# Kernel tuning notes

Measured on AMD Instinct MI355X. Metric: run time of the kernel, lower is better.

## Reference

```python
import jax, jax.numpy as jnp
import numpy as np
import math

HEAD_DIM = 128
NUM_Q_HEAD = 32
NUM_KV_HEAD = 8
WINDOW = 512
CAP = 30.0
CLIP_LO, CLIP_HI = -0.03, 1.03
EPS = 1e-5
SCALE = 1.0 / math.sqrt(HEAD_DIM)
B, S = 2, 2048


def group_rms_norm(x, w, group_size, eps):
    # x: [B, S, hidden]; normalize each contiguous group of size group_size
    Bx, Sx, H = x.shape
    ng = H // group_size
    xg = x.reshape(Bx, Sx, ng, group_size)
    inv = jax.lax.rsqrt(jnp.mean(xg * xg, axis=-1, keepdims=True) + eps)
    return (xg * inv).reshape(Bx, Sx, H) * w


def setup_inputs() -> dict:
    key = jax.random.key(0)
    kq, kk, kv, kw1, kw2 = jax.random.split(key, 5)
    q = jax.random.normal(kq, (B, S, NUM_Q_HEAD, HEAD_DIM), dtype=jnp.float32)
    k = jax.random.normal(kk, (B, S, NUM_KV_HEAD, HEAD_DIM), dtype=jnp.float32)
    v = jax.random.normal(kv, (B, S, NUM_KV_HEAD, HEAD_DIM), dtype=jnp.float32)
    # GroupRMSNorm weights, init uniform in (-1, 1)
    q_norm_w = jax.random.uniform(kw1, (NUM_Q_HEAD * HEAD_DIM,), dtype=jnp.float32, minval=-1.0, maxval=1.0)
    kv_norm_w = jax.random.uniform(kw2, (NUM_KV_HEAD * HEAD_DIM,), dtype=jnp.float32, minval=-1.0, maxval=1.0)
    return {"q": q, "k": k, "v": v, "q_norm_w": q_norm_w, "kv_norm_w": kv_norm_w}


def reference(q, k, v, q_norm_w, kv_norm_w):
    Bq, Sq, Hq, D = q.shape
    Sk = k.shape[1]
    # QK GroupRMSNorm over flattened hidden dim, group_size = head_dim
    qn = group_rms_norm(q.reshape(Bq, Sq, Hq * D), q_norm_w, HEAD_DIM, EPS).reshape(q.shape)
    kn = group_rms_norm(k.reshape(Bq, Sk, NUM_KV_HEAD * D), kv_norm_w, HEAD_DIM, EPS).reshape(k.shape)
    # GQA: repeat_interleave kv heads along head axis
    rep = Hq // NUM_KV_HEAD
    kr = jnp.repeat(kn, rep, axis=2)  # [B, Sk, Hq, D]
    vr = jnp.repeat(v, rep, axis=2)
    # scores: [B, Hq, Sq, Sk]
    scores = jnp.einsum("bqhd,bkhd->bhqk", qn, kr) * SCALE
    scores = CAP * jnp.tanh(scores / CAP)  # softmax capping
    # sliding-window + causal mask: allowed iff i - WINDOW <= j <= i (offset = Sk - Sq = 0)
    offset = Sk - Sq
    i = jnp.arange(Sq)[:, None] + offset
    j = jnp.arange(Sk)[None, :]
    allowed = (j <= i) & (j >= i - WINDOW)
    scores = jnp.where(allowed, scores, -jnp.inf)
    probs = jax.nn.softmax(scores, axis=-1)
    probs = jnp.nan_to_num(probs, nan=0.0)
    # softmax clipping
    probs = jnp.clip((CLIP_HI - CLIP_LO) * probs + CLIP_LO, 0.0, 1.0)
    out = jnp.einsum("bhqk,bkhd->bqhd", probs, vr)
    return out
```

## Files before the change

### kernel.cpp

```cpp
#include <hip/hip_runtime.h>

#define SEQ 2048
#define DD 128
#define HQ 32
#define HKV 8
#define WIN 512

typedef unsigned short u16;
typedef unsigned int u32;
typedef __attribute__((ext_vector_type(8))) short bf16x8;
typedef __attribute__((ext_vector_type(4))) float f32x4;
typedef __attribute__((ext_vector_type(2))) float f32x2;

#define SBAR() asm volatile("s_barrier" ::: "memory")
#define WAITV0() asm volatile("s_waitcnt vmcnt(0)" ::: "memory")

__device__ __forceinline__ u16 f2bf(float f) {
  u32 u = __builtin_bit_cast(u32, f);
  u += 0x7FFFu + ((u >> 16) & 1u);
  return (u16)(u >> 16);
}

__device__ __forceinline__ void gl16(const void* g, void* l) {
  __builtin_amdgcn_global_load_lds(
      (const __attribute__((address_space(1))) void*)g,
      (__attribute__((address_space(3))) void*)l, 16, 0, 0);
}

__device__ __forceinline__ u32 cvtpk(float lo, float hi) {
  u32 r;
  asm("v_cvt_pk_bf16_f32 %0, %1, %2" : "=v"(r) : "v"(lo), "v"(hi));
  return r;
}

__device__ __forceinline__ f32x2 pk_mul(f32x2 a, f32x2 b) {
  f32x2 d;
  asm("v_pk_mul_f32 %0, %1, %2" : "=v"(d) : "v"(a), "v"(b));
  return d;
}
__device__ __forceinline__ f32x2 pk_fma(f32x2 a, f32x2 b, f32x2 c) {
  f32x2 d;
  asm("v_pk_fma_f32 %0, %1, %2, %3" : "=v"(d) : "v"(a), "v"(b), "v"(c));
  return d;
}
__device__ __forceinline__ f32x2 pk_add(f32x2 a, f32x2 b) {
  f32x2 d;
  asm("v_pk_add_f32 %0, %1, %2" : "=v"(d) : "v"(a), "v"(b));
  return d;
}

__device__ __forceinline__ f32x2 score2(f32x2 x, f32x2 vL2E, f32x2 vmCE, f32x2 vmCTL) {
  f32x2 x2 = pk_mul(x, x);
  f32x2 a1 = pk_fma(x, vL2E, vmCE);
  f32x2 b1 = pk_mul(x2, vmCTL);
  return pk_fma(b1, x, a1);
}

__device__ __forceinline__ f32x2 unpk(u32 wv) {
  f32x2 r;
  r[0] = __builtin_bit_cast(float, wv << 16);
  r[1] = __builtin_bit_cast(float, wv & 0xFFFF0000u);
  return r;
}

__device__ __forceinline__ void norm_body(
    const float* __restrict__ x, const float* __restrict__ w,
    u16* __restrict__ o, int hshift, float scale, int blk, int tid) {
  const int lane = tid & 63;
  const int wv = tid >> 6;
  const int sub = lane >> 5;
  const int l5 = lane & 31;
  const int rid = blk * 8 + wv * 2 + sub;
  const int H = 1 << hshift;
  const int hh = rid & (H - 1);
  const int s = (rid >> hshift) & (SEQ - 1);
  const int b = rid >> (hshift + 11);
  const float4 xv = *(reinterpret_cast<const float4*>(x + (size_t)rid * DD) + l5);
  float ssq = xv.x * xv.x + xv.y * xv.y + xv.z * xv.z + xv.w * xv.w;
  ssq += __shfl_xor(ssq, 1);
  ssq += __shfl_xor(ssq, 2);
  ssq += __shfl_xor(ssq, 4);
  ssq += __shfl_xor(ssq, 8);
  ssq += __shfl_xor(ssq, 16);
  const float inv = rsqrtf(ssq * (1.0f / 128.0f) + 1e-5f) * scale;
  const float4 wv4 = *(reinterpret_cast<const float4*>(w + hh * DD) + l5);
  const u16 o0 = f2bf(xv.x * inv * wv4.x);
  const u16 o1 = f2bf(xv.y * inv * wv4.y);
  const u16 o2 = f2bf(xv.z * inv * wv4.z);
  const u16 o3 = f2bf(xv.w * inv * wv4.w);
  const size_t oo = (((size_t)b * H + hh) * SEQ + s) * DD + l5 * 4;
  uint2 pk;
  pk.x = (u32)o0 | ((u32)o1 << 16);
  pk.y = (u32)o2 | ((u32)o3 << 16);
  *reinterpret_cast<uint2*>(o + oo) = pk;
}

__device__ __forceinline__ void transv_body(
    const float* __restrict__ v, u16* __restrict__ vt, int bid, int t) {
  const int st = bid & 31;
  const int h = (bid >> 5) & 7;
  const int b = bid >> 8;
  const int sbase = st * 64;
  const int d = t & 127;
  const int sch = (t >> 7) * 32;
  const size_t oo = (((size_t)(b * HKV + h)) * DD + d) * SEQ + sbase + sch;
#pragma unroll
  for (int q8 = 0; q8 < 4; ++q8) {
    uint4 o;
    u32 c[4];
#pragma unroll
    for (int p = 0; p < 4; ++p) {
      const int ss0 = q8 * 8 + p * 2;
      const int s0 = sbase + sch + ss0;
      const float a0 = v[((size_t)(b * SEQ + s0) * HKV + h) * DD + d];
      const float a1 = v[((size_t)(b * SEQ + s0 + 1) * HKV + h) * DD + d];
      c[p] = (u32)f2bf(a0) | ((u32)f2bf(a1) << 16);
    }
    o.x = c[0]; o.y = c[1]; o.z = c[2]; o.w = c[3];
    *reinterpret_cast<uint4*>(vt + oo + q8 * 8) = o;
  }
}

__global__ void __launch_bounds__(256) prep_kernel(
    const float* __restrict__ q, const float* __restrict__ k,
    const float* __restrict__ v, const float* __restrict__ qw,
    const float* __restrict__ kw, u16* __restrict__ qn,
    u16* __restrict__ kn, u16* __restrict__ vt) {
  const int blk = blockIdx.x;
  const int tid = threadIdx.x;
  if (blk < 16384) {
    norm_body(q, qw, qn, 5, 0.08838834764831845f, blk, tid);
  } else if (blk < 20480) {
    norm_body(k, kw, kn, 3, 1.0f, blk - 16384, tid);
  } else {
    transv_body(v, vt, blk - 20480, tid);
  }
}

__global__ void __launch_bounds__(256, 3) attn_kernel(
    const u16* __restrict__ qn, const u16* __restrict__ kn,
    const u16* __restrict__ vt, float* __restrict__ out) {
  __shared__ char smem[32768];
  const int tid = threadIdx.x;
  const int w = tid >> 6;
  const int lane = tid & 63;
  const int c = lane & 15;
  const int g = lane >> 4;

  const int p = blockIdx.x;
  const int bid = ((p & 7) << 8) + (p >> 3);
  const int qt = (bid & 127) ^ 127;
  const int hk = (bid >> 7) & 7;
  const int b = bid >> 10;
  const int i0 = qt * 16;
  const int h = hk * 4 + w;

  const u16* qb = qn + ((size_t)(b * HQ + h) * SEQ + i0) * DD;
  const u16* kbp = kn + (size_t)(b * HKV + hk) * SEQ * DD;
  const u16* vbp = vt + (size_t)(b * HKV + hk) * DD * SEQ;

  bf16x8 aq[4];
#pragma unroll
  for (int kt = 0; kt < 4; ++kt)
    aq[kt] = *reinterpret_cast<const bf16x8*>(qb + c * DD + kt * 32 + g * 8);

  int ks = i0 - WIN;
  ks = (ks < 0) ? 0 : (ks & ~63);
  const int ntl = (i0 + 16 - ks + 63) >> 6;

  const f32x2 vL2E = {1.44269504088896f, 1.44269504088896f};
  const f32x2 vmCE = {-43.2808512266689f, -43.2808512266689f};
  const f32x2 vmCTL = {-5.343315e-4f, -5.343315e-4f};

  auto stageK = [&](int kb, int bufoff) {
    char* dst = smem + bufoff;
#pragma unroll
    for (int ci = 0; ci < 4; ++ci) {
      const int call = w * 4 + ci;
      const int row = call * 4 + g;
      const int ch = c ^ (row & 7);
      gl16(kbp + (size_t)(kb + row) * DD + ch * 8, dst + call * 1024);
    }
  };
  auto stageV = [&](int kb, int bufoff) {
    char* dst = smem + bufoff;
#pragma unroll
    for (int ci = 0; ci < 4; ++ci) {
      const int call = w * 4 + ci;
      const int vrow = call * 8 + (lane >> 3);
      const int vch = (lane & 7) ^ (vrow & 7);
      gl16(vbp + (size_t)vrow * SEQ + kb + vch * 8, dst + call * 1024);
    }
  };

  u32 ebuf[9][8];
  f32x2 lsum2 = {0.0f, 0.0f};

  stageK(ks, 0);
#pragma unroll
  for (int t = 0; t < 9; ++t) {
    if (t >= ntl) continue;
    const int kb = ks + t * 64;
    WAITV0();
    SBAR();
    if (t + 1 < ntl) stageK(kb + 64, ((t + 1) & 1) << 14);

    const char* kbuf = smem + ((t & 1) << 14);
    f32x4 sc[4] = {};
    __builtin_amdgcn_s_setprio(1);
#pragma unroll
    for (int nt = 0; nt < 4; ++nt) {
      const int jb = kb + nt * 16;
      if (jb > i0 + 15 || jb + 15 < i0 - WIN) continue;
      const int row = nt * 16 + c;
      const int sw = row & 7;
      const char* base = kbuf + row * 256;
#pragma unroll
      for (int kt = 0; kt < 4; ++kt) {
        const bf16x8 bk = *reinterpret_cast<const bf16x8*>(base + (((kt * 4 + g) ^ sw) << 4));
        sc[nt] = __builtin_amdgcn_mfma_f32_16x16x32_bf16(bk, aq[kt], sc[nt], 0, 0, 0);
      }
    }
    __builtin_amdgcn_s_setprio(0);

#pragma unroll
    for (int nt = 0; nt < 4; ++nt) {
      const int jb = kb + nt * 16;
      if (jb > i0 + 15 || jb + 15 < i0 - WIN) {
        ebuf[t][nt * 2] = 0;
        ebuf[t][nt * 2 + 1] = 0;
        continue;
      }
      const bool needmask = (jb + 15 > i0) || (jb < i0 + 15 - WIN);
      f32x2 lo = __builtin_shufflevector(sc[nt], sc[nt], 0, 1);
      f32x2 hi = __builtin_shufflevector(sc[nt], sc[nt], 2, 3);
      const f32x2 a0 = score2(lo, vL2E, vmCE, vmCTL);
      const f32x2 a1 = score2(hi, vL2E, vmCE, vmCTL);
      float e0 = __builtin_amdgcn_exp2f(a0[0]);
      float e1 = __builtin_amdgcn_exp2f(a0[1]);
      float e2 = __builtin_amdgcn_exp2f(a1[0]);
      float e3 = __builtin_amdgcn_exp2f(a1[1]);
      if (needmask) {
        const int difg = i0 + c - jb - g * 4;
        e0 = ((u32)(difg - 0) <= WIN) ? e0 : 0.0f;
        e1 = ((u32)(difg - 1) <= WIN) ? e1 : 0.0f;
        e2 = ((u32)(difg - 2) <= WIN) ? e2 : 0.0f;
        e3 = ((u32)(difg - 3) <= WIN) ? e3 : 0.0f;
      }
      ebuf[t][nt * 2] = cvtpk(e0, e1);
      ebuf[t][nt * 2 + 1] = cvtpk(e2, e3);
      const f32x2 eA = {e0, e1};
      const f32x2 eB = {e2, e3};
      lsum2 = pk_add(lsum2, pk_add(eA, eB));
    }
  }
  WAITV0();
  SBAR();

  stageV(ks, 0);

  float l = lsum2[0] + lsum2[1];
  l += __shfl_xor(l, 16);
  l += __shfl_xor(l, 32);
  const float ar = 1.06f / l;
  const f32x2 var2 = {ar, ar};
  const f32x2 vm003 = {-0.03f, -0.03f};

  f32x4 acc[8] = {};

#pragma unroll
  for (int t = 0; t < 9; ++t) {
    if (t >= ntl) continue;
    const int kb = ks + t * 64;
    WAITV0();
    SBAR();
    if (t + 1 < ntl) stageV(kb + 64, ((t + 1) & 1) << 14);
    const char* ldsV = smem + ((t & 1) << 14);

#pragma unroll
    for (int k2 = 0; k2 < 2; ++k2) {
      const int jb2 = kb + k2 * 32;
      if (jb2 > i0 + 15 || jb2 + 31 < i0 - WIN) continue;

      u32 cw[4];
#pragma unroll
      for (int u = 0; u < 4; ++u) {
        const f32x2 ef = unpk(ebuf[t][k2 * 4 + u]);
        const f32x2 pr = pk_fma(ef, var2, vm003);
        cw[u] = cvtpk(__builtin_amdgcn_fmed3f(pr[0], 0.0f, 1.0f),
                      __builtin_amdgcn_fmed3f(pr[1], 0.0f, 1.0f));
      }

      union PU { bf16x8 v; u32 w4[4]; };
      PU pf;
      {
        u32 x0 = cw[0], y0 = cw[2];
        asm("v_permlane32_swap_b32 %0, %1" : "+v"(x0), "+v"(y0));
        asm("v_permlane16_swap_b32 %0, %1" : "+v"(x0), "+v"(y0));
        u32 x1 = cw[1], y1 = cw[3];
        asm("v_permlane32_swap_b32 %0, %1" : "+v"(x1), "+v"(y1));
        asm("v_permlane16_swap_b32 %0, %1" : "+v"(x1), "+v"(y1));
        pf.w4[0] = x0;
        pf.w4[1] = x1;
        pf.w4[2] = y0;
        pf.w4[3] = y1;
      }

      __builtin_amdgcn_s_setprio(1);
#pragma unroll
      for (int dt = 0; dt < 8; ++dt) {
        const int rv = dt * 16 + c;
        const bf16x8 bv = *reinterpret_cast<const bf16x8*>(
            ldsV + rv * 128 + (((k2 * 4 + g) ^ (rv & 7)) << 4));
        acc[dt] = __builtin_amdgcn_mfma_f32_16x16x32_bf16(pf.v, bv, acc[dt], 0, 0, 0);
      }
      __builtin_amdgcn_s_setprio(0);
    }
  }

#pragma unroll
  for (int r = 0; r < 4; ++r) {
    const int i = i0 + g * 4 + r;
    float* op = out + (((size_t)b * SEQ + i) * HQ + h) * DD + c;
#pragma unroll
    for (int dt = 0; dt < 8; ++dt) op[dt * 16] = acc[dt][r];
  }
}

extern "C" void kernel_launch(void* const* d_in, const int* in_sizes, int n_in,
                              void* d_out, int out_size, void* d_ws, size_t ws_size,
                              hipStream_t stream) {
  const float* q = (const float*)d_in[0];
  const float* k = (const float*)d_in[1];
  const float* v = (const float*)d_in[2];
  const float* qw = (const float*)d_in[3];
  const float* kw = (const float*)d_in[4];
  float* out = (float*)d_out;

  u16* qn = (u16*)d_ws;
  u16* kn = qn + (size_t)2 * HQ * SEQ * DD;
  u16* vt = kn + (size_t)2 * HKV * SEQ * DD;

  prep_kernel<<<20992, 256, 0, stream>>>(q, k, v, qw, kw, qn, kn, vt);
  attn_kernel<<<2048, 256, 0, stream>>>(qn, kn, vt, out);
}
```

Measured before the change: 93.55 us.

## Fuse Q RMS norm into attention kernel, drop Q prep pass

Q group RMS normalization and bf16 conversion move from the prep kernel into the attention kernel's prologue. Each wave loads fp32 Q rows directly, reduces the sum of squares with shuffles, applies weight and softmax scale, and packs the result into MFMA operands. This removes the 16M-element Q write and re-read through workspace and shrinks the prep grid. In exchange the attention kernel reads twice the bytes for Q with a strided layout and does extra ALU work in its prologue, which overlaps with the first K stage load.

```diff
diff --git a/kernel.cpp b/kernel.cpp
--- a/kernel.cpp
+++ b/kernel.cpp
@@ -65,7 +65,7 @@
 
 __device__ __forceinline__ void norm_body(
     const float* __restrict__ x, const float* __restrict__ w,
-    u16* __restrict__ o, int hshift, float scale, int blk, int tid) {
+    u16* __restrict__ o, int hshift, int blk, int tid) {
   const int lane = tid & 63;
   const int wv = tid >> 6;
   const int sub = lane >> 5;
@@ -82,7 +82,7 @@
   ssq += __shfl_xor(ssq, 4);
   ssq += __shfl_xor(ssq, 8);
   ssq += __shfl_xor(ssq, 16);
-  const float inv = rsqrtf(ssq * (1.0f / 128.0f) + 1e-5f) * scale;
+  const float inv = rsqrtf(ssq * (1.0f / 128.0f) + 1e-5f);
   const float4 wv4 = *(reinterpret_cast<const float4*>(w + hh * DD) + l5);
   const u16 o0 = f2bf(xv.x * inv * wv4.x);
   const u16 o1 = f2bf(xv.y * inv * wv4.y);
@@ -122,24 +122,21 @@
 }
 
 __global__ void __launch_bounds__(256) prep_kernel(
-    const float* __restrict__ q, const float* __restrict__ k,
-    const float* __restrict__ v, const float* __restrict__ qw,
-    const float* __restrict__ kw, u16* __restrict__ qn,
-    u16* __restrict__ kn, u16* __restrict__ vt) {
+    const float* __restrict__ k, const float* __restrict__ v,
+    const float* __restrict__ kw, u16* __restrict__ kn, u16* __restrict__ vt) {
   const int blk = blockIdx.x;
   const int tid = threadIdx.x;
-  if (blk < 16384) {
-    norm_body(q, qw, qn, 5, 0.08838834764831845f, blk, tid);
-  } else if (blk < 20480) {
-    norm_body(k, kw, kn, 3, 1.0f, blk - 16384, tid);
+  if (blk < 4096) {
+    norm_body(k, kw, kn, 3, blk, tid);
   } else {
-    transv_body(v, vt, blk - 20480, tid);
+    transv_body(v, vt, blk - 4096, tid);
   }
 }
 
 __global__ void __launch_bounds__(256, 3) attn_kernel(
-    const u16* __restrict__ qn, const u16* __restrict__ kn,
-    const u16* __restrict__ vt, float* __restrict__ out) {
+    const float* __restrict__ q32, const float* __restrict__ qw,
+    const u16* __restrict__ kn, const u16* __restrict__ vt,
+    float* __restrict__ out) {
   __shared__ char smem[32768];
   const int tid = threadIdx.x;
   const int w = tid >> 6;
@@ -155,22 +152,12 @@
   const int i0 = qt * 16;
   const int h = hk * 4 + w;
 
-  const u16* qb = qn + ((size_t)(b * HQ + h) * SEQ + i0) * DD;
   const u16* kbp = kn + (size_t)(b * HKV + hk) * SEQ * DD;
   const u16* vbp = vt + (size_t)(b * HKV + hk) * DD * SEQ;
-
-  bf16x8 aq[4];
-#pragma unroll
-  for (int kt = 0; kt < 4; ++kt)
-    aq[kt] = *reinterpret_cast<const bf16x8*>(qb + c * DD + kt * 32 + g * 8);
 
   int ks = i0 - WIN;
   ks = (ks < 0) ? 0 : (ks & ~63);
   const int ntl = (i0 + 16 - ks + 63) >> 6;
-
-  const f32x2 vL2E = {1.44269504088896f, 1.44269504088896f};
-  const f32x2 vmCE = {-43.2808512266689f, -43.2808512266689f};
-  const f32x2 vmCTL = {-5.343315e-4f, -5.343315e-4f};
 
   auto stageK = [&](int kb, int bufoff) {
     char* dst = smem + bufoff;
@@ -193,10 +180,47 @@
     }
   };
 
+  stageK(ks, 0);
+
+  union AQ { bf16x8 v; u32 w4[4]; };
+  AQ aq[4];
+  {
+    const float* qf = q32 + (((size_t)b * SEQ + i0 + c) * HQ + h) * DD;
+    const float* wf = qw + h * DD;
+    float xv[4][8];
+    float ss = 0.0f;
+#pragma unroll
+    for (int kt = 0; kt < 4; ++kt) {
+      const float4 a0 = *reinterpret_cast<const float4*>(qf + kt * 32 + g * 8);
+      const float4 a1 = *reinterpret_cast<const float4*>(qf + kt * 32 + g * 8 + 4);
+      xv[kt][0] = a0.x; xv[kt][1] = a0.y; xv[kt][2] = a0.z; xv[kt][3] = a0.w;
+      xv[kt][4] = a1.x; xv[kt][5] = a1.y; xv[kt][6] = a1.z; xv[kt][7] = a1.w;
+      ss = fmaf(a0.x, a0.x, ss); ss = fmaf(a0.y, a0.y, ss);
+      ss = fmaf(a0.z, a0.z, ss); ss = fmaf(a0.w, a0.w, ss);
+      ss = fmaf(a1.x, a1.x, ss); ss = fmaf(a1.y, a1.y, ss);
+      ss = fmaf(a1.z, a1.z, ss); ss = fmaf(a1.w, a1.w, ss);
+    }
+    ss += __shfl_xor(ss, 16);
+    ss += __shfl_xor(ss, 32);
+    const float inv = rsqrtf(ss * (1.0f / 128.0f) + 1e-5f) * 0.08838834764831845f;
+#pragma unroll
+    for (int kt = 0; kt < 4; ++kt) {
+      const float4 w0 = *reinterpret_cast<const float4*>(wf + kt * 32 + g * 8);
+      const float4 w1 = *reinterpret_cast<const float4*>(wf + kt * 32 + g * 8 + 4);
+      aq[kt].w4[0] = cvtpk(xv[kt][0] * inv * w0.x, xv[kt][1] * inv * w0.y);
+      aq[kt].w4[1] = cvtpk(xv[kt][2] * inv * w0.z, xv[kt][3] * inv * w0.w);
+      aq[kt].w4[2] = cvtpk(xv[kt][4] * inv * w1.x, xv[kt][5] * inv * w1.y);
+      aq[kt].w4[3] = cvtpk(xv[kt][6] * inv * w1.z, xv[kt][7] * inv * w1.w);
+    }
+  }
+
+  const f32x2 vL2E = {1.44269504088896f, 1.44269504088896f};
+  const f32x2 vmCE = {-43.2808512266689f, -43.2808512266689f};
+  const f32x2 vmCTL = {-5.343315e-4f, -5.343315e-4f};
+
   u32 ebuf[9][8];
   f32x2 lsum2 = {0.0f, 0.0f};
 
-  stageK(ks, 0);
 #pragma unroll
   for (int t = 0; t < 9; ++t) {
     if (t >= ntl) continue;
@@ -218,7 +242,7 @@
 #pragma unroll
       for (int kt = 0; kt < 4; ++kt) {
         const bf16x8 bk = *reinterpret_cast<const bf16x8*>(base + (((kt * 4 + g) ^ sw) << 4));
-        sc[nt] = __builtin_amdgcn_mfma_f32_16x16x32_bf16(bk, aq[kt], sc[nt], 0, 0, 0);
+        sc[nt] = __builtin_amdgcn_mfma_f32_16x16x32_bf16(bk, aq[kt].v, sc[nt], 0, 0, 0);
       }
     }
     __builtin_amdgcn_s_setprio(0);
@@ -337,10 +361,9 @@
   const float* kw = (const float*)d_in[4];
   float* out = (float*)d_out;
 
-  u16* qn = (u16*)d_ws;
-  u16* kn = qn + (size_t)2 * HQ * SEQ * DD;
+  u16* kn = (u16*)d_ws;
   u16* vt = kn + (size_t)2 * HKV * SEQ * DD;
 
-  prep_kernel<<<20992, 256, 0, stream>>>(q, k, v, qw, kw, qn, kn, vt);
-  attn_kernel<<<2048, 256, 0, stream>>>(qn, kn, vt, out);
-}
+  prep_kernel<<<4608, 256, 0, stream>>>(k, v, kw, kn, vt);
+  attn_kernel<<<2048, 256, 0, stream>>>(q, qw, kn, vt, out);
+}
```

Measured after the change: 86.42 us. 7.6% less time.
